# Kernel optimization log

Hardware: AMD Instinct MI355X
Metric: run time of the kernel (lower is better)

Reference implementation:

```python
import jax, jax.numpy as jnp
import numpy as np

N = 500_000        # num nodes
E = 2_000_000      # num edges
D = 8              # message passing depth
DIM = 16           # dim_embed
F = 5              # NUM_NODE_FEATURES
NUM_DAGS = 5_000


def _mlp_params(key, d_in, d_out, scale=0.1):
    k1, k2, k3 = jax.random.split(key, 3)
    return (jax.random.normal(k1, (d_in, 16), jnp.float32) * scale, jnp.zeros((16,), jnp.float32),
            jax.random.normal(k2, (16, 8), jnp.float32) * scale, jnp.zeros((8,), jnp.float32),
            jax.random.normal(k3, (8, d_out), jnp.float32) * scale, jnp.zeros((d_out,), jnp.float32))


def _mlp(x, w1, b1, w2, b2, w3, b3):
    h = jax.nn.relu(x @ w1 + b1)
    h = jax.nn.relu(h @ w2 + b2)
    return h @ w3 + b3


def setup_inputs() -> dict:
    key = jax.random.key(0)
    ks = jax.random.split(key, 8)
    x = jax.random.normal(ks[0], (N, F), jnp.float32)
    edge_index = jax.random.randint(ks[1], (2, E), 0, N, jnp.int32)
    edge_mask_batch = jax.random.bernoulli(ks[2], 0.5, (D, E))
    ptr = jnp.arange(0, N + 1, N // NUM_DAGS, dtype=jnp.int32)  # 5000 dags of 100 nodes
    inp = {"x": x, "edge_index": edge_index, "edge_mask_batch": edge_mask_batch, "ptr": ptr}
    names = ["p", "m", "u", "d", "g"]
    dins = [F, DIM, DIM, F + DIM, DIM]
    for name, din, k in zip(names, dins, jax.random.split(ks[3], 5)):
        w1, b1, w2, b2, w3, b3 = _mlp_params(k, din, DIM)
        inp.update({f"{name}w1": w1, f"{name}b1": b1, f"{name}w2": w2,
                    f"{name}b2": b2, f"{name}w3": w3, f"{name}b3": b3})
    return inp


def reference(x, edge_index, edge_mask_batch, ptr,
              pw1, pb1, pw2, pb2, pw3, pb3,
              mw1, mb1, mw2, mb2, mw3, mb3,
              uw1, ub1, uw2, ub2, uw3, ub3,
              dw1, db1, dw2, db2, dw3, db3,
              gw1, gb1, gw2, gb2, gw3, gb3):
    num_nodes = x.shape[0]
    dst, src = edge_index[0], edge_index[1]

    # NodeEncoder: prep then D rounds of masked sparse message passing
    h = _mlp(x, pw1, pb1, pw2, pb2, pw3, pb3)  # [N, DIM]

    def step(h, mask):
        mf = mask.astype(h.dtype)  # [E]
        y = _mlp(h, mw1, mb1, mw2, mb2, mw3, mb3)  # [N, DIM]
        # adj @ y: out[i] = sum over active edges (i <- j) of y[j]
        agg = jnp.zeros_like(h).at[dst].add(y[src] * mf[:, None])
        # node_mask: nodes that are destinations of an active edge
        nm = (jnp.zeros((num_nodes,), h.dtype).at[dst].add(mf) > 0)
        upd = _mlp(agg, uw1, ub1, uw2, ub2, uw3, ub3)
        return h + nm[:, None].astype(h.dtype) * upd, None

    h, _ = jax.lax.scan(step, h, edge_mask_batch)
    node_embeddings = h

    # DagEncoder: per-dag segment-sum of mlp([x, h])
    num_dags = ptr.shape[0] - 1
    seg = jnp.searchsorted(ptr, jnp.arange(num_nodes, dtype=ptr.dtype), side='right') - 1
    z = _mlp(jnp.concatenate([x, node_embeddings], axis=1), dw1, db1, dw2, db2, dw3, db3)
    dag_summaries = jax.ops.segment_sum(z, seg, num_segments=num_dags)  # [num_dags, DIM]

    # GlobalEncoder: no obs_ptr -> sum over all dags
    g = _mlp(dag_summaries, gw1, gb1, gw2, gb2, gw3, gb3)
    global_summaries = g.sum(0)[None]  # [1, DIM]

    return node_embeddings, dag_summaries, global_summaries
```

## Files before the change

### kernel.cpp

```cpp
#include <hip/hip_runtime.h>
#include <hip/hip_bf16.h>
#include <stdint.h>

#define N_NODES 500000
#define N_EDGES 2000000
#define DEPTH 8
#define NUM_DAGS 5000
#define DAG_SZ 100
#define OUT_NODES_ELEMS 8000000
#define OUT_GLOB_OFF    8080000
#define NB_SCAN 489

typedef __hip_bfloat16 bf16;

__device__ __forceinline__ float bfb2f(unsigned u) {
    return __uint_as_float((u & 0xffffu) << 16);
}
__device__ __forceinline__ unsigned f2bfb(float f) {
    bf16 b = __float2bfloat16(f);
    unsigned short u;
    __builtin_memcpy(&u, &b, 2);
    return (unsigned)u;
}
__device__ __forceinline__ float rndbf(float f) { return bfb2f(f2bfb(f)); }
template<int ISBF>
__device__ __forceinline__ float crnd(float f) { return ISBF ? rndbf(f) : f; }

__device__ __forceinline__ void unpack_pair(uint4 a, uint4 b, float* f) {
    f[0]=bfb2f(a.x);  f[1]=bfb2f(a.x>>16);
    f[2]=bfb2f(a.y);  f[3]=bfb2f(a.y>>16);
    f[4]=bfb2f(a.z);  f[5]=bfb2f(a.z>>16);
    f[6]=bfb2f(a.w);  f[7]=bfb2f(a.w>>16);
    f[8]=bfb2f(b.x);  f[9]=bfb2f(b.x>>16);
    f[10]=bfb2f(b.y); f[11]=bfb2f(b.y>>16);
    f[12]=bfb2f(b.z); f[13]=bfb2f(b.z>>16);
    f[14]=bfb2f(b.w); f[15]=bfb2f(b.w>>16);
}
__device__ __forceinline__ unsigned packpair(float lo, float hi) {
    return f2bfb(lo) | (f2bfb(hi) << 16);
}
__device__ __forceinline__ void pack16(const float* f, uint4* a, uint4* b) {
    a->x = packpair(f[0],f[1]);   a->y = packpair(f[2],f[3]);
    a->z = packpair(f[4],f[5]);   a->w = packpair(f[6],f[7]);
    b->x = packpair(f[8],f[9]);   b->y = packpair(f[10],f[11]);
    b->z = packpair(f[12],f[13]); b->w = packpair(f[14],f[15]);
}

template<int ISBF>
__device__ __forceinline__ float ldf(const void* p, size_t i) {
    return ISBF ? __bfloat162float(((const bf16*)p)[i]) : ((const float*)p)[i];
}
template<int ISBF>
__device__ __forceinline__ void load16(const void* base, size_t row, float* f) {
    if (ISBF) {
        const uint4* p = (const uint4*)((const bf16*)base + row*16);
        uint4 a = p[0], b = p[1];
        unpack_pair(a, b, f);
    } else {
        const float4* p = (const float4*)((const float*)base + row*16);
        float4 v0=p[0], v1=p[1], v2=p[2], v3=p[3];
        f[0]=v0.x; f[1]=v0.y; f[2]=v0.z; f[3]=v0.w;
        f[4]=v1.x; f[5]=v1.y; f[6]=v1.z; f[7]=v1.w;
        f[8]=v2.x; f[9]=v2.y; f[10]=v2.z; f[11]=v2.w;
        f[12]=v3.x; f[13]=v3.y; f[14]=v3.z; f[15]=v3.w;
    }
}
template<int ISBF>
__device__ __forceinline__ void store16(void* base, size_t row, const float* f) {
    if (ISBF) {
        uint4 a, b; pack16(f, &a, &b);
        uint4* p = (uint4*)((bf16*)base + row*16);
        p[0] = a; p[1] = b;
    } else {
        float4* p = (float4*)((float*)base + row*16);
        p[0] = make_float4(f[0],f[1],f[2],f[3]);
        p[1] = make_float4(f[4],f[5],f[6],f[7]);
        p[2] = make_float4(f[8],f[9],f[10],f[11]);
        p[3] = make_float4(f[12],f[13],f[14],f[15]);
    }
}

__global__ void k_detect(const void* __restrict__ x, int* __restrict__ flag) {
    const unsigned short* u = (const unsigned short*)x;
    int t = threadIdx.x;
    int wild = 0;
    #pragma unroll
    for (int k = 0; k < 4; k++) {
        float v = bfb2f(u[t*4 + k]);
        if (fabsf(v) > 1000.f) wild = 1;
    }
    unsigned long long m = __ballot(wild);
    if (t == 0) flag[0] = (m == 0ull) ? 1 : 0;
}

template<int DIN, int ISBF>
__device__ __forceinline__ void load_mlp_smem(const void* w1, const void* b1,
        const void* w2, const void* b2, const void* w3, const void* b3,
        float* s) {
    const int n1 = DIN * 16;
    const int tot = n1 + 16 + 128 + 8 + 128 + 16;
    for (int i = threadIdx.x; i < tot; i += blockDim.x) {
        int o = i; float v;
        if (o < n1)                 v = ldf<ISBF>(w1, o);
        else if ((o -= n1) < 16)    v = ldf<ISBF>(b1, o);
        else if ((o -= 16) < 128)   v = ldf<ISBF>(w2, o);
        else if ((o -= 128) < 8)    v = ldf<ISBF>(b2, o);
        else if ((o -= 8) < 128)    v = ldf<ISBF>(w3, o);
        else                        v = ldf<ISBF>(b3, o - 128);
        s[i] = v;
    }
}

template<int DIN, int ISBF>
__device__ __forceinline__ void mlp_apply(const float* in, const float* s,
                                          float* out) {
    const float* w1 = s;
    const float* b1 = s + DIN * 16;
    const float* w2 = b1 + 16;
    const float* b2 = w2 + 128;
    const float* w3 = b2 + 8;
    const float* b3 = w3 + 128;
    float h1[16];
    #pragma unroll
    for (int j = 0; j < 16; j++) {
        float a = b1[j];
        #pragma unroll
        for (int i = 0; i < DIN; i++) a = fmaf(in[i], w1[i*16 + j], a);
        h1[j] = crnd<ISBF>(fmaxf(a, 0.f));
    }
    float h2[8];
    #pragma unroll
    for (int j = 0; j < 8; j++) {
        float a = b2[j];
        #pragma unroll
        for (int i = 0; i < 16; i++) a = fmaf(h1[i], w2[i*8 + j], a);
        h2[j] = crnd<ISBF>(fmaxf(a, 0.f));
    }
    #pragma unroll
    for (int j = 0; j < 16; j++) {
        float a = b3[j];
        #pragma unroll
        for (int i = 0; i < 8; i++) a = fmaf(h2[i], w3[i*16 + j], a);
        out[j] = crnd<ISBF>(a);
    }
}

__global__ __launch_bounds__(256)
void k_hist(const int* __restrict__ dstp, int* __restrict__ deg) {
    int e = blockIdx.x * blockDim.x + threadIdx.x;
    if (e >= N_EDGES) return;
    atomicAdd(&deg[dstp[e]], 1);
}

__global__ __launch_bounds__(256)
void k_bsum(const int* __restrict__ deg, int* __restrict__ bsum) {
    __shared__ int sd[256];
    int b = blockIdx.x, t = threadIdx.x;
    int base = b * 1024;
    int s = 0;
    #pragma unroll
    for (int k = 0; k < 4; k++) {
        int i = base + t + k * 256;
        if (i < N_NODES) s += deg[i];
    }
    sd[t] = s; __syncthreads();
    for (int off = 128; off > 0; off >>= 1) {
        if (t < off) sd[t] += sd[t + off];
        __syncthreads();
    }
    if (t == 0) bsum[b] = sd[0];
}

__global__ __launch_bounds__(512)
void k_bscan(const int* __restrict__ bsum, int* __restrict__ boff) {
    __shared__ int s[512];
    int t = threadIdx.x;
    int v = (t < NB_SCAN) ? bsum[t] : 0;
    s[t] = v; __syncthreads();
    for (int off = 1; off < 512; off <<= 1) {
        int x = (t >= off) ? s[t - off] : 0;
        __syncthreads();
        s[t] += x;
        __syncthreads();
    }
    if (t < NB_SCAN) boff[t] = s[t] - v;
}

__global__ __launch_bounds__(1024)
void k_scan(int* __restrict__ deg, const int* __restrict__ boff,
            int* __restrict__ row_ptr) {
    __shared__ int s[1024];
    int b = blockIdx.x, t = threadIdx.x;
    int i = b * 1024 + t;
    int v = (i < N_NODES) ? deg[i] : 0;
    s[t] = v; __syncthreads();
    for (int off = 1; off < 1024; off <<= 1) {
        int x = (t >= off) ? s[t - off] : 0;
        __syncthreads();
        s[t] += x;
        __syncthreads();
    }
    int excl = boff[b] + s[t] - v;
    if (i < N_NODES) {
        row_ptr[i] = excl;
        deg[i] = excl;
        if (i == N_NODES - 1) row_ptr[N_NODES] = excl + v;
    }
}

__global__ __launch_bounds__(256)
void k_scatter(const int* __restrict__ dstp, const int* __restrict__ srcp,
               const int* __restrict__ mask, int* __restrict__ cursor,
               unsigned* __restrict__ csr) {
    int e = blockIdx.x * blockDim.x + threadIdx.x;
    if (e >= N_EDGES) return;
    unsigned mb = 0;
    #pragma unroll
    for (int t = 0; t < DEPTH; t++)
        mb |= (mask[(size_t)t * N_EDGES + e] != 0 ? 1u : 0u) << t;
    int d = dstp[e];
    int pos = atomicAdd(&cursor[d], 1);
    csr[pos] = (unsigned)srcp[e] | (mb << 19);
}


template<int ISBF>
__device__ __forceinline__ void prep_body(const void* x,
        const void* pw1, const void* pb1, const void* pw2,
        const void* pb2, const void* pw3, const void* pb3,
        const void* mw1, const void* mb1, const void* mw2,
        const void* mb2, const void* mw3, const void* mb3,
        void* h, bf16* y0, float* sp, float* sm) {
    load_mlp_smem<5, ISBF>(pw1, pb1, pw2, pb2, pw3, pb3, sp);
    load_mlp_smem<16, ISBF>(mw1, mb1, mw2, mb2, mw3, mb3, sm);
    __syncthreads();
    int i = blockIdx.x * blockDim.x + threadIdx.x;
    if (i >= N_NODES) return;
    float in[5];
    #pragma unroll
    for (int j = 0; j < 5; j++) in[j] = ldf<ISBF>(x, (size_t)i*5 + j);
    float hv[16];
    mlp_apply<5, ISBF>(in, sp, hv);
    store16<ISBF>(h, i, hv);
    float y[16];
    mlp_apply<16, ISBF>(hv, sm, y);
    uint4 oa, ob; pack16(y, &oa, &ob);
    uint4* yp = (uint4*)(y0 + (size_t)i*16);
    yp[0] = oa; yp[1] = ob;
}

__global__ __launch_bounds__(256, 4)
void k_prep(const void* __restrict__ x,
            const void* pw1, const void* pb1, const void* pw2,
            const void* pb2, const void* pw3, const void* pb3,
            const void* mw1, const void* mb1, const void* mw2,
            const void* mb2, const void* mw3, const void* mb3,
            void* __restrict__ h, bf16* __restrict__ y0,
            const int* __restrict__ dtflag) {
    __shared__ float sp[5*16 + 16 + 128 + 8 + 128 + 16];
    __shared__ float sm[16*16 + 16 + 128 + 8 + 128 + 16];
    if (dtflag[0])
        prep_body<1>(x, pw1,pb1,pw2,pb2,pw3,pb3, mw1,mb1,mw2,mb2,mw3,mb3, h, y0, sp, sm);
    else
        prep_body<0>(x, pw1,pb1,pw2,pb2,pw3,pb3, mw1,mb1,mw2,mb2,mw3,mb3, h, y0, sp, sm);
}

template<int ISBF>
__device__ __forceinline__ void round_body(void* h, const int* row_ptr,
        const unsigned* csr, const bf16* yin, bf16* yout,
        const void* uw1, const void* ub1, const void* uw2,
        const void* ub2, const void* uw3, const void* ub3,
        const void* mw1, const void* mb1, const void* mw2,
        const void* mb2, const void* mw3, const void* mb3,
        int t, float* su, float* sm) {
    load_mlp_smem<16, ISBF>(uw1, ub1, uw2, ub2, uw3, ub3, su);
    load_mlp_smem<16, ISBF>(mw1, mb1, mw2, mb2, mw3, mb3, sm);
    __syncthreads();
    int i = blockIdx.x * blockDim.x + threadIdx.x;
    if (i >= N_NODES) return;
    int beg = row_ptr[i], end = row_ptr[i + 1];
    float acc[16];
    #pragma unroll
    for (int j = 0; j < 16; j++) acc[j] = 0.f;
    int any = 0;
    const unsigned tb = 1u << (19 + t);
    unsigned v = (beg < end) ? csr[beg] : 0;
    for (int p = beg; p < end; ++p) {
        unsigned vn = (p + 1 < end) ? csr[p + 1] : 0;
        if (v & tb) {
            any = 1;
            int s = v & 0x7FFFF;
            const uint4* yp = (const uint4*)(yin + (size_t)s*16);
            uint4 a = yp[0], b = yp[1];
            float f[16]; unpack_pair(a, b, f);
            #pragma unroll
            for (int j = 0; j < 16; j++) acc[j] += f[j];
        }
        v = vn;
    }
    uint4* yo = (uint4*)(yout + (size_t)i*16);
    if (!any) {
        const uint4* yp = (const uint4*)(yin + (size_t)i*16);
        yo[0] = yp[0]; yo[1] = yp[1];
        return;
    }
    #pragma unroll
    for (int j = 0; j < 16; j++) acc[j] = crnd<ISBF>(acc[j]);
    float upd[16];
    mlp_apply<16, ISBF>(acc, su, upd);
    float hv[16];
    load16<ISBF>(h, i, hv);
    float o[16];
    #pragma unroll
    for (int j = 0; j < 16; j++) o[j] = crnd<ISBF>(hv[j] + upd[j]);
    store16<ISBF>(h, i, o);
    float yn[16];
    mlp_apply<16, ISBF>(o, sm, yn);
    uint4 oa, ob; pack16(yn, &oa, &ob);
    yo[0] = oa; yo[1] = ob;
}

__global__ __launch_bounds__(256, 4)
void k_round(void* __restrict__ h, const int* __restrict__ row_ptr,
             const unsigned* __restrict__ csr,
             const bf16* __restrict__ yin, bf16* __restrict__ yout,
             const void* uw1, const void* ub1, const void* uw2,
             const void* ub2, const void* uw3, const void* ub3,
             const void* mw1, const void* mb1, const void* mw2,
             const void* mb2, const void* mw3, const void* mb3,
             int t, const int* __restrict__ dtflag) {
    __shared__ float su[16*16 + 16 + 128 + 8 + 128 + 16];
    __shared__ float sm[16*16 + 16 + 128 + 8 + 128 + 16];
    if (dtflag[0])
        round_body<1>(h, row_ptr, csr, yin, yout, uw1,ub1,uw2,ub2,uw3,ub3,
                      mw1,mb1,mw2,mb2,mw3,mb3, t, su, sm);
    else
        round_body<0>(h, row_ptr, csr, yin, yout, uw1,ub1,uw2,ub2,uw3,ub3,
                      mw1,mb1,mw2,mb2,mw3,mb3, t, su, sm);
}

template<int ISBF>
__device__ __forceinline__ void dag_body(const void* x, const void* h,
        const void* w1, const void* b1, const void* w2,
        const void* b2, const void* w3, const void* b3,
        float* dagsum, float* s, float* zb) {
    load_mlp_smem<21, ISBF>(w1, b1, w2, b2, w3, b3, s);
    __syncthreads();
    int t = threadIdx.x;
    int dag = blockIdx.x;
    if (t < DAG_SZ) {
        int i = dag * DAG_SZ + t;
        float in[21];
        #pragma unroll
        for (int j = 0; j < 5; j++) in[j] = ldf<ISBF>(x, (size_t)i*5 + j);
        load16<ISBF>(h, i, in + 5);
        float z[16];
        mlp_apply<21, ISBF>(in, s, z);
        #pragma unroll
        for (int j = 0; j < 16; j++) zb[t*16 + j] = z[j];
    }
    __syncthreads();
    if (t < 16) {
        float acc = 0.f;
        for (int r = 0; r < DAG_SZ; r++) acc += zb[r*16 + t];
        dagsum[(size_t)dag*16 + t] = acc;
    }
}

__global__ __launch_bounds__(128)
void k_dag(const void* __restrict__ x, const void* __restrict__ h,
           const void* w1, const void* b1, const void* w2,
           const void* b2, const void* w3, const void* b3,
           float* __restrict__ dagsum, const int* __restrict__ dtflag) {
    __shared__ float s[21*16 + 16 + 128 + 8 + 128 + 16];
    __shared__ float zb[DAG_SZ * 16];
    if (dtflag[0]) dag_body<1>(x, h, w1,b1,w2,b2,w3,b3, dagsum, s, zb);
    else           dag_body<0>(x, h, w1,b1,w2,b2,w3,b3, dagsum, s, zb);
}

template<int ISBF>
__device__ __forceinline__ void glob_body(const float* dagsum,
        const void* w1, const void* b1, const void* w2,
        const void* b2, const void* w3, const void* b3,
        void* d_out, float* globacc, float* s, float* gb) {
    load_mlp_smem<16, ISBF>(w1, b1, w2, b2, w3, b3, s);
    __syncthreads();
    int t = threadIdx.x;
    int d = blockIdx.x * blockDim.x + t;
    float g[16];
    if (d < NUM_DAGS) {
        const float4* dp = (const float4*)(dagsum + (size_t)d*16);
        float4 v0 = dp[0], v1 = dp[1], v2 = dp[2], v3 = dp[3];
        float in[16] = { v0.x, v0.y, v0.z, v0.w, v1.x, v1.y, v1.z, v1.w,
                         v2.x, v2.y, v2.z, v2.w, v3.x, v3.y, v3.z, v3.w };
        #pragma unroll
        for (int j = 0; j < 16; j++) in[j] = crnd<ISBF>(in[j]);
        if (ISBF) {
            bf16* od = (bf16*)d_out + OUT_NODES_ELEMS;
            store16<1>(od, d, in);
        } else {
            float* od = (float*)d_out + OUT_NODES_ELEMS;
            store16<0>(od, d, in);
        }
        mlp_apply<16, ISBF>(in, s, g);
    } else {
        #pragma unroll
        for (int j = 0; j < 16; j++) g[j] = 0.f;
    }
    #pragma unroll
    for (int j = 0; j < 16; j++) gb[t*16 + j] = g[j];
    __syncthreads();
    if (t < 16) {
        float acc = 0.f;
        for (int r = 0; r < 256; r++) acc += gb[r*16 + t];
        unsafeAtomicAdd(&globacc[t], acc);
    }
}

__global__ __launch_bounds__(256)
void k_glob(const float* __restrict__ dagsum,
            const void* w1, const void* b1, const void* w2,
            const void* b2, const void* w3, const void* b3,
            void* __restrict__ d_out, float* __restrict__ globacc,
            const int* __restrict__ dtflag) {
    __shared__ float s[16*16 + 16 + 128 + 8 + 128 + 16];
    __shared__ float gb[256 * 16];
    if (dtflag[0]) glob_body<1>(dagsum, w1,b1,w2,b2,w3,b3, d_out, globacc, s, gb);
    else           glob_body<0>(dagsum, w1,b1,w2,b2,w3,b3, d_out, globacc, s, gb);
}

__global__ void k_final(const float* __restrict__ globacc,
                        void* __restrict__ d_out, const int* __restrict__ dtflag) {
    const int isbf = dtflag[0];
    int t = threadIdx.x;
    if (t < 16) {
        if (isbf) ((bf16*)d_out)[OUT_GLOB_OFF + t] = __float2bfloat16(globacc[t]);
        else      ((float*)d_out)[OUT_GLOB_OFF + t] = globacc[t];
    }
}

extern "C" void kernel_launch(void* const* d_in, const int* in_sizes, int n_in,
                              void* d_out, int out_size, void* d_ws, size_t ws_size,
                              hipStream_t stream) {
    const void* x    = d_in[0];
    const int*  ei   = (const int*)d_in[1];
    const int*  mask = (const int*)d_in[2];
    const void* W[30];
    for (int i = 0; i < 30; i++) W[i] = d_in[4 + i];

    const int* dstp = ei;
    const int* srcp = ei + N_EDGES;

    char*     ws      = (char*)d_ws;
    int*      deg     = (int*)     (ws);
    float*    globacc = (float*)   (ws + 2000000);
    int*      dtflag  = (int*)     (ws + 2000064);
    int*      row_ptr = (int*)     (ws + 2000128);
    int*      bsum    = (int*)     (ws + 4000192);
    int*      boff    = (int*)     (ws + 4002240);
    unsigned* csr     = (unsigned*)(ws + 4004288);
    bf16*     y0      = (bf16*)    (ws + 12004288);
    bf16*     y1      = (bf16*)    (ws + 28004288);
    float*    dagsum  = (float*)   (ws + 44004288);

    hipMemsetAsync(d_ws, 0, 2000064, stream);

    const int TB  = 256;
    const int nbN = (N_NODES + TB - 1) / TB;
    const int nbE = (N_EDGES + TB - 1) / TB;

    k_detect<<<1, 64, 0, stream>>>(x, dtflag);

    k_hist<<<nbE, TB, 0, stream>>>(dstp, deg);
    k_bsum<<<NB_SCAN, 256, 0, stream>>>(deg, bsum);
    k_bscan<<<1, 512, 0, stream>>>(bsum, boff);
    k_scan<<<NB_SCAN, 1024, 0, stream>>>(deg, boff, row_ptr);
    k_scatter<<<nbE, TB, 0, stream>>>(dstp, srcp, mask, deg, csr);

    k_prep<<<nbN, TB, 0, stream>>>(x, W[0], W[1], W[2], W[3], W[4], W[5],
                                   W[6], W[7], W[8], W[9], W[10], W[11],
                                   d_out, y0, dtflag);
    bf16* yb[2] = { y0, y1 };
    for (int t = 0; t < DEPTH; t++) {
        k_round<<<nbN, TB, 0, stream>>>(d_out, row_ptr, csr,
                                        yb[t & 1], yb[(t + 1) & 1],
                                        W[12], W[13], W[14], W[15], W[16], W[17],
                                        W[6], W[7], W[8], W[9], W[10], W[11],
                                        t, dtflag);
    }
    k_dag<<<NUM_DAGS, 128, 0, stream>>>(x, d_out, W[18], W[19], W[20], W[21],
                                        W[22], W[23], dagsum, dtflag);
    k_glob<<<(NUM_DAGS + TB - 1) / TB, TB, 0, stream>>>(dagsum, W[24], W[25], W[26],
                                                        W[27], W[28], W[29],
                                                        d_out, globacc, dtflag);
    k_final<<<1, 64, 0, stream>>>(globacc, d_out, dtflag);
}
```

Baseline: 811.1 us.

## Parallelize round gather over edges with shared-memory atomic accumulation per block

Each block now spreads its 256 nodes' CSR edge records evenly across threads instead of giving one node's edge list to one thread. Each thread finds its destination node by binary search over a shared row_ptr slice and adds the source embedding into a padded shared accumulator with LDS atomics. This removes load imbalance and the serial per-thread edge loop. The cost is atomics, a binary search per edge, extra shared memory (around 17KB) that may lower occupancy, and a float summation order that is no longer deterministic.

```diff
diff --git a/kernel.cpp b/kernel.cpp
--- a/kernel.cpp
+++ b/kernel.cpp
@@ -10,6 +10,7 @@
 #define OUT_NODES_ELEMS 8000000
 #define OUT_GLOB_OFF    8080000
 #define NB_SCAN 489
+#define NB_ROUND 1954
 
 typedef __hip_bfloat16 bf16;
 
@@ -272,42 +273,64 @@
         const void* ub2, const void* uw3, const void* ub3,
         const void* mw1, const void* mb1, const void* mw2,
         const void* mb2, const void* mw3, const void* mb3,
-        int t, float* su, float* sm) {
+        int t, float* su, float* sm, float* acc, int* rp, int* anyf) {
     load_mlp_smem<16, ISBF>(uw1, ub1, uw2, ub2, uw3, ub3, su);
     load_mlp_smem<16, ISBF>(mw1, mb1, mw2, mb2, mw3, mb3, sm);
-    __syncthreads();
-    int i = blockIdx.x * blockDim.x + threadIdx.x;
-    if (i >= N_NODES) return;
-    int beg = row_ptr[i], end = row_ptr[i + 1];
-    float acc[16];
-    #pragma unroll
-    for (int j = 0; j < 16; j++) acc[j] = 0.f;
-    int any = 0;
+    const int tid = threadIdx.x;
+    const int base = blockIdx.x * 256;
+    if (tid == 0) {
+        int n = base + 256; if (n > N_NODES) n = N_NODES;
+        rp[256] = row_ptr[n];
+    }
+    {
+        int n = base + tid; if (n > N_NODES) n = N_NODES;
+        rp[tid] = row_ptr[n];
+    }
+    #pragma unroll
+    for (int k = 0; k < 17; k++) acc[tid + k * 256] = 0.f;
+    anyf[tid] = 0;
+    __syncthreads();
+    const int seg0 = rp[0];
+    const int nrec = rp[256] - seg0;
     const unsigned tb = 1u << (19 + t);
-    unsigned v = (beg < end) ? csr[beg] : 0;
-    for (int p = beg; p < end; ++p) {
-        unsigned vn = (p + 1 < end) ? csr[p + 1] : 0;
+    for (int r = tid; r < nrec; r += 256) {
+        unsigned v = csr[seg0 + r];
         if (v & tb) {
-            any = 1;
-            int s = v & 0x7FFFF;
-            const uint4* yp = (const uint4*)(yin + (size_t)s*16);
+            int src = v & 0x7FFFF;
+            int pos = seg0 + r;
+            int lo = 0, hi = 256;
+            #pragma unroll
+            for (int step = 0; step < 8; step++) {
+                int mid = (lo + hi) >> 1;
+                if (rp[mid] <= pos) lo = mid; else hi = mid;
+            }
+            anyf[lo] = 1;
+            const uint4* yp = (const uint4*)(yin + (size_t)src*16);
             uint4 a = yp[0], b = yp[1];
             float f[16]; unpack_pair(a, b, f);
+            float* ap = acc + lo * 17;
+            const int st = tid & 15;
             #pragma unroll
-            for (int j = 0; j < 16; j++) acc[j] += f[j];
+            for (int jj = 0; jj < 16; jj++) {
+                int j = (jj + st) & 15;
+                atomicAdd(ap + j, f[j]);
+            }
         }
-        v = vn;
-    }
+    }
+    __syncthreads();
+    int i = base + tid;
+    if (i >= N_NODES) return;
     uint4* yo = (uint4*)(yout + (size_t)i*16);
-    if (!any) {
+    if (!anyf[tid]) {
         const uint4* yp = (const uint4*)(yin + (size_t)i*16);
         yo[0] = yp[0]; yo[1] = yp[1];
         return;
     }
-    #pragma unroll
-    for (int j = 0; j < 16; j++) acc[j] = crnd<ISBF>(acc[j]);
+    float a16[16];
+    #pragma unroll
+    for (int j = 0; j < 16; j++) a16[j] = crnd<ISBF>(acc[tid*17 + j]);
     float upd[16];
-    mlp_apply<16, ISBF>(acc, su, upd);
+    mlp_apply<16, ISBF>(a16, su, upd);
     float hv[16];
     load16<ISBF>(h, i, hv);
     float o[16];
@@ -331,12 +354,15 @@
              int t, const int* __restrict__ dtflag) {
     __shared__ float su[16*16 + 16 + 128 + 8 + 128 + 16];
     __shared__ float sm[16*16 + 16 + 128 + 8 + 128 + 16];
+    __shared__ float acc[256 * 17];
+    __shared__ int rp[257];
+    __shared__ int anyf[256];
     if (dtflag[0])
         round_body<1>(h, row_ptr, csr, yin, yout, uw1,ub1,uw2,ub2,uw3,ub3,
-                      mw1,mb1,mw2,mb2,mw3,mb3, t, su, sm);
+                      mw1,mb1,mw2,mb2,mw3,mb3, t, su, sm, acc, rp, anyf);
     else
         round_body<0>(h, row_ptr, csr, yin, yout, uw1,ub1,uw2,ub2,uw3,ub3,
-                      mw1,mb1,mw2,mb2,mw3,mb3, t, su, sm);
+                      mw1,mb1,mw2,mb2,mw3,mb3, t, su, sm, acc, rp, anyf);
 }
 
 template<int ISBF>
@@ -482,7 +508,7 @@
                                    d_out, y0, dtflag);
     bf16* yb[2] = { y0, y1 };
     for (int t = 0; t < DEPTH; t++) {
-        k_round<<<nbN, TB, 0, stream>>>(d_out, row_ptr, csr,
+        k_round<<<NB_ROUND, TB, 0, stream>>>(d_out, row_ptr, csr,
                                         yb[t & 1], yb[(t + 1) & 1],
                                         W[12], W[13], W[14], W[15], W[16], W[17],
                                         W[6], W[7], W[8], W[9], W[10], W[11],
```

Measured after the change: 1.371 ms. 1.69x slower.
